# Performance work log

Measured on AMD Instinct MI355X. Metric: run time of the kernel, lower is better.

## Reference

```python
import jax, jax.numpy as jnp
import numpy as np

N = 100000   # total nodes (types a: [0,50000), b: [50000,100000))
E = 500000   # edges per edge type
T = 4        # number of edge types
D_IN = 128
H = 4        # heads
F = 32       # out_feats per head
NEG_SLOPE = 0.2


def setup_inputs() -> dict:
    key = jax.random.key(0)
    ks = jax.random.split(key, 8)
    feat = jax.random.normal(ks[0], (N, D_IN), dtype=jnp.float32)
    src = jax.random.randint(ks[1], (T, E), 0, N)
    dst = jax.random.randint(ks[2], (T, E), 0, N)
    is_b = jnp.arange(N) >= (N // 2)  # node-type mask (type2mask)
    W = jax.random.normal(ks[3], (T, D_IN, H * F), dtype=jnp.float32) * (1.0 / np.sqrt(D_IN))
    attn_l = jax.random.normal(ks[4], (T, H, F), dtype=jnp.float32) * 0.1
    attn_r = jax.random.normal(ks[5], (T, H, F), dtype=jnp.float32) * 0.1
    W_merge = jax.random.normal(ks[6], (2 * H * F, F), dtype=jnp.float32) * (1.0 / np.sqrt(2 * H * F))
    b_merge = jax.random.normal(ks[7], (F,), dtype=jnp.float32) * 0.01
    return {"feat": feat, "src": src, "dst": dst, "is_b": is_b,
            "W": W, "attn_l": attn_l, "attn_r": attn_r,
            "W_merge": W_merge, "b_merge": b_merge}


def _gat_etype(feat, src_t, dst_t, W_t, al_t, ar_t):
    # Projected features: [N, H, F]
    ft = (feat @ W_t).reshape(N, H, F)
    el = jnp.einsum('nhf,hf->nh', ft, al_t)  # [N, H]
    er = jnp.einsum('nhf,hf->nh', ft, ar_t)  # [N, H]
    # u_add_v then LeakyReLU: [E, H]
    e = el[src_t] + er[dst_t]
    e = jnp.where(e > 0, e, NEG_SLOPE * e)
    # edge_softmax over incoming edges of each dst node (stable)
    m = jax.lax.stop_gradient(jax.ops.segment_max(e, dst_t, num_segments=N))
    ex = jnp.exp(e - m[dst_t])
    denom = jax.ops.segment_sum(ex, dst_t, num_segments=N)
    a = ex / denom[dst_t]  # [E, H]
    # u_mul_e + scatter-sum: [N, H, F]
    msg = ft[src_t] * a[:, :, None]
    out = jax.ops.segment_sum(msg, dst_t, num_segments=N)
    return out.reshape(N, H * F)


def reference(feat, src, dst, is_b, W, attn_l, attn_r, W_merge, b_merge):
    outs = [_gat_etype(feat, src[t], dst[t], W[t], attn_l[t], attn_r[t])
            for t in range(T)]
    # etypes dst order: a, a, b, b -> two per-etype feats per dst ntype
    feat_a = jnp.concatenate([outs[0], outs[1]], axis=1) @ W_merge + b_merge  # [N, F]
    feat_b = jnp.concatenate([outs[2], outs[3]], axis=1) @ W_merge + b_merge  # [N, F]
    # base_aggr_func: start with type-a result, overwrite type-b rows
    return jnp.where(is_b[:, None], feat_b, feat_a)
```

## Files before the change

kernel.cpp:

```cpp
#include <hip/hip_runtime.h>
#include <hip/hip_fp16.h>

typedef short short8 __attribute__((ext_vector_type(8)));
typedef _Float16 half8 __attribute__((ext_vector_type(8)));
typedef float f32x4 __attribute__((ext_vector_type(4)));

#define N_NODES 100000
#define N_A     50000
#define N_EDGES 500000
#define N_T     4
#define D_IN    128
#define HF      128
#define BCOLS   144
#define TN      (N_T * N_NODES)
#define TE      (N_T * N_EDGES)
#define NB1     ((TN + 1023) / 1024)
#define TILE_E  (BCOLS * D_IN)
#define LOG2E   1.44269504088896340736f
#define NPROJB  1563
#define NHISTB  ((TE + 255) / 256)

__device__ __forceinline__ unsigned short f2b(float f) {
  unsigned int u = __float_as_uint(f);
  u += 0x7FFFu + ((u >> 16) & 1u);
  return (unsigned short)(u >> 16);
}
__device__ __forceinline__ unsigned int pkh(float lo, float hi) {
  auto v = __builtin_amdgcn_cvt_pkrtz(lo, hi);
  unsigned int u; __builtin_memcpy(&u, &v, 4); return u;
}
__device__ __forceinline__ unsigned short f2h(float f) {
  auto v = __builtin_amdgcn_cvt_pkrtz(f, 0.f);
  unsigned int u; __builtin_memcpy(&u, &v, 4); return (unsigned short)(u & 0xFFFFu);
}
__device__ __forceinline__ __half2 w2h(unsigned int u) {
  __half2 h; __builtin_memcpy(&h, &u, 4); return h;
}
__device__ __forceinline__ unsigned int h2w(__half2 h) {
  unsigned int u; __builtin_memcpy(&u, &h, 4); return u;
}

__global__ __launch_bounds__(256) void k_prep(const float* __restrict__ W,
    const float* __restrict__ al, const float* __restrict__ ar,
    const float* __restrict__ Wm,
    unsigned short* __restrict__ Bt, unsigned short* __restrict__ WmT)
{
  if (blockIdx.x < 2) {
    int idx = blockIdx.x * 256 + threadIdx.x;
    int t = idx >> 7, k = idx & 127;
    const float* Wr = W + ((size_t)t * D_IN + k) * HF;
    unsigned short* o = Bt + (size_t)t * TILE_E;
    for (int j = 0; j < HF; ++j)
      o[(j * D_IN + k) ^ ((j & 7) << 3)] = f2b(Wr[j]);
    for (int h = 0; h < 4; ++h) {
      float sl = 0.f, sr = 0.f;
      const float* alh = al + (t * 4 + h) * 32;
      const float* arh = ar + (t * 4 + h) * 32;
      for (int f = 0; f < 32; ++f) { float w = Wr[h * 32 + f]; sl += w * alh[f]; sr += w * arh[f]; }
      int jl = 128 + h, jr = 132 + h;
      o[(jl * D_IN + k) ^ ((jl & 7) << 3)] = f2b(sl * LOG2E);
      o[(jr * D_IN + k) ^ ((jr & 7) << 3)] = f2b(sr * LOG2E);
    }
    for (int j = 136; j < 144; ++j)
      o[(j * D_IN + k) ^ ((j & 7) << 3)] = 0;
  } else {
    int idx = (blockIdx.x - 2) * 256 + threadIdx.x;
    int kidx = idx >> 5, j = idx & 31;
    int slot = kidx >> 7, p = kidx & 127;
    int col = (p & 7) * 16 + (p >> 3);
    WmT[j * 256 + kidx] = f2h(Wm[(slot * 128 + col) * 32 + j]);
  }
}

__global__ __launch_bounds__(256, 4) void k_projhist(const float* __restrict__ feat,
    const unsigned short* __restrict__ Btg,
    unsigned short* __restrict__ ftg,
    float* __restrict__ elg, float* __restrict__ erg,
    const int* __restrict__ dst, int* __restrict__ cnt, int* __restrict__ rank)
{
  if (blockIdx.x >= NPROJB) {
    int idx = (blockIdx.x - NPROJB) * 256 + threadIdx.x;
    if (idx >= TE) return;
    int t = idx / N_EDGES;
    int d = dst[idx];
    bool keep = (t < 2) ? (d < N_A) : (d >= N_A);
    if (keep) rank[idx] = atomicAdd(&cnt[t * N_NODES + d], 1);
    return;
  }
  __shared__ __align__(16) unsigned short Bs[TILE_E];
  const int tid = threadIdx.x;
  const int wave = tid >> 6, lane = tid & 63;
  const int l15 = lane & 15, g = lane >> 4;
  const int wrow0 = blockIdx.x * 64 + wave * 16;

  short8 a[4];
  {
    int row = wrow0 + l15;
    const float* fr = feat + (size_t)(row < N_NODES ? row : N_NODES - 1) * D_IN;
#pragma unroll
    for (int kt = 0; kt < 4; ++kt) {
      float4 v0 = *(const float4*)(fr + kt * 32 + g * 8);
      float4 v1 = *(const float4*)(fr + kt * 32 + g * 8 + 4);
      short8 s;
      s[0] = (short)f2b(v0.x); s[1] = (short)f2b(v0.y);
      s[2] = (short)f2b(v0.z); s[3] = (short)f2b(v0.w);
      s[4] = (short)f2b(v1.x); s[5] = (short)f2b(v1.y);
      s[6] = (short)f2b(v1.z); s[7] = (short)f2b(v1.w);
      a[kt] = s;
    }
  }

  for (int t = 0; t < N_T; ++t) {
    if (t > 0) __syncthreads();
    {
      const uint4* src = (const uint4*)(Btg + (size_t)t * TILE_E);
      uint4* dstv = (uint4*)Bs;
#pragma unroll
      for (int i = 0; i < 9; ++i)
        dstv[i * 256 + tid] = src[i * 256 + tid];
    }
    __syncthreads();

    f32x4 acc[8];
#pragma unroll
    for (int ct = 0; ct < 8; ++ct) {
      f32x4 c = {0.f, 0.f, 0.f, 0.f};
#pragma unroll
      for (int kt = 0; kt < 4; ++kt) {
        int row = ct * 16 + l15;
        int boff = (row * 256 + kt * 64 + g * 16) ^ ((l15 & 7) << 4);
        short8 b = *(const short8*)((const char*)Bs + boff);
        c = __builtin_amdgcn_mfma_f32_16x16x32_bf16(a[kt], b, c, 0, 0, 0);
      }
      acc[ct] = c;
    }
    {
      f32x4 c8 = {0.f, 0.f, 0.f, 0.f};
#pragma unroll
      for (int kt = 0; kt < 4; ++kt) {
        int row = 128 + l15;
        int boff = (row * 256 + kt * 64 + g * 16) ^ ((l15 & 7) << 4);
        short8 b = *(const short8*)((const char*)Bs + boff);
        c8 = __builtin_amdgcn_mfma_f32_16x16x32_bf16(a[kt], b, c8, 0, 0, 0);
      }
      if (l15 < 8) {
#pragma unroll
        for (int r = 0; r < 4; ++r) {
          int row = wrow0 + g * 4 + r;
          if (row < N_NODES) {
            float v = c8[r];
            if (l15 < 4) elg[((size_t)t * N_NODES + row) * 4 + l15] = v;
            else         erg[((size_t)t * N_NODES + row) * 4 + (l15 - 4)] = v;
          }
        }
      }
    }
#pragma unroll
    for (int r = 0; r < 4; ++r) {
      int row = wrow0 + g * 4 + r;
      if (row < N_NODES) {
        uint4 o;
        o.x = pkh(acc[0][r], acc[1][r]);
        o.y = pkh(acc[2][r], acc[3][r]);
        o.z = pkh(acc[4][r], acc[5][r]);
        o.w = pkh(acc[6][r], acc[7][r]);
        *(uint4*)(ftg + ((size_t)t * N_NODES + row) * HF + l15 * 8) = o;
      }
    }
  }
}

__global__ __launch_bounds__(256) void k_scan1(const int* __restrict__ cnt,
    int* __restrict__ ofs, int* __restrict__ bsum) {
  __shared__ int ts[256];
  int b = blockIdx.x, t = threadIdx.x;
  int base = b * 1024 + t * 4;
  int v0 = 0, v1 = 0, v2 = 0, v3 = 0;
  if (base + 0 < TN) v0 = cnt[base + 0];
  if (base + 1 < TN) v1 = cnt[base + 1];
  if (base + 2 < TN) v2 = cnt[base + 2];
  if (base + 3 < TN) v3 = cnt[base + 3];
  int s = v0 + v1 + v2 + v3;
  ts[t] = s;
  __syncthreads();
  for (int o = 1; o < 256; o <<= 1) {
    int x = (t >= o) ? ts[t - o] : 0;
    __syncthreads();
    ts[t] += x;
    __syncthreads();
  }
  int run = ts[t] - s;
  if (base + 0 < TN) ofs[base + 0] = run; run += v0;
  if (base + 1 < TN) ofs[base + 1] = run; run += v1;
  if (base + 2 < TN) ofs[base + 2] = run; run += v2;
  if (base + 3 < TN) ofs[base + 3] = run;
  if (t == 255) bsum[b] = ts[255];
}

__global__ __launch_bounds__(512) void k_scan2(int* __restrict__ bsum) {
  __shared__ int ts[512];
  int t = threadIdx.x;
  int v = (t < NB1) ? bsum[t] : 0;
  ts[t] = v;
  __syncthreads();
  for (int o = 1; o < 512; o <<= 1) {
    int x = (t >= o) ? ts[t - o] : 0;
    __syncthreads();
    ts[t] += x;
    __syncthreads();
  }
  if (t < NB1) bsum[t] = ts[t] - v;
}

__global__ __launch_bounds__(256) void k_scatter(const int* __restrict__ src, const int* __restrict__ dst,
    const int* __restrict__ ofs, const int* __restrict__ bsum, const int* __restrict__ rank,
    int* __restrict__ bkt) {
  int idx = blockIdx.x * 256 + threadIdx.x;
  if (idx >= TE) return;
  int t = idx / N_EDGES;
  int d = dst[idx];
  bool keep = (t < 2) ? (d < N_A) : (d >= N_A);
  if (!keep) return;
  int key = t * N_NODES + d;
  int p = ofs[key] + bsum[key >> 10] + rank[idx];
  bkt[p] = t * N_NODES + src[idx];
}

__global__ __launch_bounds__(256) void k_gather(const int* __restrict__ bkt,
    const int* __restrict__ ofs, const int* __restrict__ cnt, const int* __restrict__ bsum,
    const float* __restrict__ elg, const float* __restrict__ erg,
    const uint4* __restrict__ ftu, uint4* __restrict__ aggb)
{
  int wid = blockIdx.x * 4 + (threadIdx.x >> 6);
  int lane = threadIdx.x & 63;
  int g8 = lane >> 3, l7 = lane & 7;
  int pid = wid * 8 + g8;
  int n = pid >> 1, slot = pid & 1;
  int t = slot + ((n >= N_A) ? 2 : 0);
  int key = t * N_NODES + n;
  int base = ofs[key] + bsum[key >> 10];
  int c = cnt[key];
  float4 er4 = *(const float4*)(erg + (size_t)key * 4);
  __half2 A0 = __float2half2_rn(0.f), A1 = A0, A2 = A0, A3 = A0;
  __half2 B0 = A0, B1 = A0, B2 = A0, B3 = A0;
  float d0 = 0.f, d1 = 0.f, d2 = 0.f, d3 = 0.f;
  int qb = l7 * 2;
  for (int i = 0; i < c; i += 4) {
    bool v1 = i + 1 < c, v2 = i + 2 < c, v3 = i + 3 < c;
    int e0 = base + i;
    int e1 = base + (v1 ? i + 1 : i);
    int e2 = base + (v2 ? i + 2 : i);
    int e3 = base + (v3 ? i + 3 : i);
    int s0 = bkt[e0], s1 = bkt[e1], s2 = bkt[e2], s3 = bkt[e3];
    float4 eA = *(const float4*)(elg + (size_t)s0 * 4);
    float4 eB = *(const float4*)(elg + (size_t)s1 * 4);
    float4 eC = *(const float4*)(elg + (size_t)s2 * 4);
    float4 eD = *(const float4*)(elg + (size_t)s3 * 4);
    uint4 u0a = ftu[(size_t)s0 * 16 + qb], u0b = ftu[(size_t)s0 * 16 + qb + 1];
    uint4 u1a = ftu[(size_t)s1 * 16 + qb], u1b = ftu[(size_t)s1 * 16 + qb + 1];
    uint4 u2a = ftu[(size_t)s2 * 16 + qb], u2b = ftu[(size_t)s2 * 16 + qb + 1];
    uint4 u3a = ftu[(size_t)s3 * 16 + qb], u3b = ftu[(size_t)s3 * 16 + qb + 1];
    float s;
    float wa0, wa1, wa2, wa3, wb0, wb1, wb2, wb3;
    float wc0, wc1, wc2, wc3, wd0, wd1, wd2, wd3;
    s = eA.x + er4.x; wa0 = exp2f(fmaxf(s, 0.2f * s));
    s = eA.y + er4.y; wa1 = exp2f(fmaxf(s, 0.2f * s));
    s = eA.z + er4.z; wa2 = exp2f(fmaxf(s, 0.2f * s));
    s = eA.w + er4.w; wa3 = exp2f(fmaxf(s, 0.2f * s));
    s = eB.x + er4.x; wb0 = exp2f(fmaxf(s, 0.2f * s));
    s = eB.y + er4.y; wb1 = exp2f(fmaxf(s, 0.2f * s));
    s = eB.z + er4.z; wb2 = exp2f(fmaxf(s, 0.2f * s));
    s = eB.w + er4.w; wb3 = exp2f(fmaxf(s, 0.2f * s));
    s = eC.x + er4.x; wc0 = exp2f(fmaxf(s, 0.2f * s));
    s = eC.y + er4.y; wc1 = exp2f(fmaxf(s, 0.2f * s));
    s = eC.z + er4.z; wc2 = exp2f(fmaxf(s, 0.2f * s));
    s = eC.w + er4.w; wc3 = exp2f(fmaxf(s, 0.2f * s));
    s = eD.x + er4.x; wd0 = exp2f(fmaxf(s, 0.2f * s));
    s = eD.y + er4.y; wd1 = exp2f(fmaxf(s, 0.2f * s));
    s = eD.z + er4.z; wd2 = exp2f(fmaxf(s, 0.2f * s));
    s = eD.w + er4.w; wd3 = exp2f(fmaxf(s, 0.2f * s));
    if (!v1) { wb0 = wb1 = wb2 = wb3 = 0.f; }
    if (!v2) { wc0 = wc1 = wc2 = wc3 = 0.f; }
    if (!v3) { wd0 = wd1 = wd2 = wd3 = 0.f; }
    d0 += wa0 + wb0 + wc0 + wd0;
    d1 += wa1 + wb1 + wc1 + wd1;
    d2 += wa2 + wb2 + wc2 + wd2;
    d3 += wa3 + wb3 + wc3 + wd3;
    __half2 h0, h1, h2, h3;
    h0 = __float2half2_rn(wa0); h1 = __float2half2_rn(wa1);
    h2 = __float2half2_rn(wa2); h3 = __float2half2_rn(wa3);
    A0 = __hfma2(w2h(u0a.x), h0, A0); A1 = __hfma2(w2h(u0a.y), h1, A1);
    A2 = __hfma2(w2h(u0a.z), h2, A2); A3 = __hfma2(w2h(u0a.w), h3, A3);
    B0 = __hfma2(w2h(u0b.x), h0, B0); B1 = __hfma2(w2h(u0b.y), h1, B1);
    B2 = __hfma2(w2h(u0b.z), h2, B2); B3 = __hfma2(w2h(u0b.w), h3, B3);
    h0 = __float2half2_rn(wb0); h1 = __float2half2_rn(wb1);
    h2 = __float2half2_rn(wb2); h3 = __float2half2_rn(wb3);
    A0 = __hfma2(w2h(u1a.x), h0, A0); A1 = __hfma2(w2h(u1a.y), h1, A1);
    A2 = __hfma2(w2h(u1a.z), h2, A2); A3 = __hfma2(w2h(u1a.w), h3, A3);
    B0 = __hfma2(w2h(u1b.x), h0, B0); B1 = __hfma2(w2h(u1b.y), h1, B1);
    B2 = __hfma2(w2h(u1b.z), h2, B2); B3 = __hfma2(w2h(u1b.w), h3, B3);
    h0 = __float2half2_rn(wc0); h1 = __float2half2_rn(wc1);
    h2 = __float2half2_rn(wc2); h3 = __float2half2_rn(wc3);
    A0 = __hfma2(w2h(u2a.x), h0, A0); A1 = __hfma2(w2h(u2a.y), h1, A1);
    A2 = __hfma2(w2h(u2a.z), h2, A2); A3 = __hfma2(w2h(u2a.w), h3, A3);
    B0 = __hfma2(w2h(u2b.x), h0, B0); B1 = __hfma2(w2h(u2b.y), h1, B1);
    B2 = __hfma2(w2h(u2b.z), h2, B2); B3 = __hfma2(w2h(u2b.w), h3, B3);
    h0 = __float2half2_rn(wd0); h1 = __float2half2_rn(wd1);
    h2 = __float2half2_rn(wd2); h3 = __float2half2_rn(wd3);
    A0 = __hfma2(w2h(u3a.x), h0, A0); A1 = __hfma2(w2h(u3a.y), h1, A1);
    A2 = __hfma2(w2h(u3a.z), h2, A2); A3 = __hfma2(w2h(u3a.w), h3, A3);
    B0 = __hfma2(w2h(u3b.x), h0, B0); B1 = __hfma2(w2h(u3b.y), h1, B1);
    B2 = __hfma2(w2h(u3b.z), h2, B2); B3 = __hfma2(w2h(u3b.w), h3, B3);
  }
  __half2 i0 = __float2half2_rn((c > 0) ? 1.f / d0 : 0.f);
  __half2 i1 = __float2half2_rn((c > 0) ? 1.f / d1 : 0.f);
  __half2 i2 = __float2half2_rn((c > 0) ? 1.f / d2 : 0.f);
  __half2 i3 = __float2half2_rn((c > 0) ? 1.f / d3 : 0.f);
  uint4 oA, oB;
  oA.x = h2w(__hmul2(A0, i0)); oA.y = h2w(__hmul2(A1, i1));
  oA.z = h2w(__hmul2(A2, i2)); oA.w = h2w(__hmul2(A3, i3));
  oB.x = h2w(__hmul2(B0, i0)); oB.y = h2w(__hmul2(B1, i1));
  oB.z = h2w(__hmul2(B2, i2)); oB.w = h2w(__hmul2(B3, i3));
  size_t ob = (size_t)n * 32 + slot * 16 + qb;
  aggb[ob] = oA;
  aggb[ob + 1] = oB;
}

__global__ __launch_bounds__(256) void k_merge(const unsigned short* __restrict__ aggb,
    const unsigned short* __restrict__ WmT, const float* __restrict__ bm,
    float* __restrict__ out)
{
  __shared__ __align__(16) unsigned short Al[64 * 264];
  __shared__ __align__(16) unsigned short Bl[32 * 264];
  int n0 = blockIdx.x * 64;
  int tid = threadIdx.x;
  const uint4* asrc = (const uint4*)(aggb + (size_t)n0 * 256);
  for (int i = tid; i < 2048; i += 256) {
    int r = i >> 5, c = i & 31;
    *(uint4*)&Al[r * 264 + c * 8] = asrc[r * 32 + c];
  }
  for (int i = tid; i < 1024; i += 256) {
    int r = i >> 5, c = i & 31;
    *(uint4*)&Bl[r * 264 + c * 8] = ((const uint4*)WmT)[r * 32 + c];
  }
  __syncthreads();
  int wave = tid >> 6, lane = tid & 63;
  int l15 = lane & 15, lk = (lane >> 4) * 8;
  half8 a[8];
#pragma unroll
  for (int kt = 0; kt < 8; ++kt)
    a[kt] = *(const half8*)&Al[(wave * 16 + l15) * 264 + kt * 32 + lk];
  f32x4 acc0 = {0.f, 0.f, 0.f, 0.f}, acc1 = {0.f, 0.f, 0.f, 0.f};
#pragma unroll
  for (int kt = 0; kt < 8; ++kt) {
    half8 b0 = *(const half8*)&Bl[l15 * 264 + kt * 32 + lk];
    half8 b1 = *(const half8*)&Bl[(16 + l15) * 264 + kt * 32 + lk];
    acc0 = __builtin_amdgcn_mfma_f32_16x16x32_f16(a[kt], b0, acc0, 0, 0, 0);
    acc1 = __builtin_amdgcn_mfma_f32_16x16x32_f16(a[kt], b1, acc1, 0, 0, 0);
  }
  float bm0 = bm[l15], bm1 = bm[16 + l15];
#pragma unroll
  for (int r = 0; r < 4; ++r) {
    int row = n0 + wave * 16 + (lane >> 4) * 4 + r;
    if (row < N_NODES) {
      out[(size_t)row * 32 + l15] = acc0[r] + bm0;
      out[(size_t)row * 32 + 16 + l15] = acc1[r] + bm1;
    }
  }
}

extern "C" void kernel_launch(void* const* d_in, const int* in_sizes, int n_in,
                              void* d_out, int out_size, void* d_ws, size_t ws_size,
                              hipStream_t stream)
{
  const float* feat = (const float*)d_in[0];
  const int*   src  = (const int*)d_in[1];
  const int*   dst  = (const int*)d_in[2];
  const float* W    = (const float*)d_in[4];
  const float* al   = (const float*)d_in[5];
  const float* ar   = (const float*)d_in[6];
  const float* Wm   = (const float*)d_in[7];
  const float* bm   = (const float*)d_in[8];
  float* out = (float*)d_out;
  (void)in_sizes; (void)n_in; (void)out_size; (void)ws_size;

  char* w = (char*)d_ws;
  size_t o = 0;
  auto take = [&](size_t bytes) -> void* {
    void* p = w + o;
    o += (bytes + 255) & ~(size_t)255;
    return p;
  };
  unsigned short* Btg = (unsigned short*)take((size_t)N_T * TILE_E * 2);
  unsigned short* WmT = (unsigned short*)take((size_t)32 * 256 * 2);
  unsigned short* ftg = (unsigned short*)take((size_t)N_T * N_NODES * HF * 2);
  float* elg   = (float*)take((size_t)N_T * N_NODES * 4 * 4);
  float* erg   = (float*)take((size_t)N_T * N_NODES * 4 * 4);
  int*   cntb  = (int*)take((size_t)TN * 4);
  int*   ofs   = (int*)take((size_t)TN * 4);
  int*   bsum  = (int*)take(4096);
  int*   rank  = (int*)take((size_t)TE * 4);
  int*   bkt   = (int*)take((size_t)TE * 4);
  unsigned short* aggb = (unsigned short*)take((size_t)(N_NODES + 64) * 256 * 2);

  hipMemsetAsync(cntb, 0, (size_t)TN * 4, stream);

  k_prep<<<34, 256, 0, stream>>>(W, al, ar, Wm, Btg, WmT);
  k_projhist<<<NPROJB + NHISTB, 256, 0, stream>>>(feat, Btg, ftg, elg, erg, dst, cntb, rank);
  k_scan1<<<NB1, 256, 0, stream>>>(cntb, ofs, bsum);
  k_scan2<<<1, 512, 0, stream>>>(bsum);
  k_scatter<<<(TE + 255) / 256, 256, 0, stream>>>(src, dst, ofs, bsum, rank, bkt);
  k_gather<<<6250, 256, 0, stream>>>(bkt, ofs, cntb, bsum, elg, erg, (const uint4*)ftg, (uint4*)aggb);
  k_merge<<<1563, 256, 0, stream>>>(aggb, WmT, bm, out);
}
```

Before: 197.2 us.

## Fuse merge GEMM into gather kernel and split projection from histogram

The merge matmul now runs inside the gather kernel. Each block stages its 16 aggregated node rows in LDS and two waves apply the merge MFMA with weights read directly from global memory, so the intermediate aggregate buffer is never written or reread. The combined projection/histogram launch is split into two separate kernels. This gives up the overlap between the two and leaves half the waves idle during the merge step.

```diff
diff --git a/kernel.cpp b/kernel.cpp
--- a/kernel.cpp
+++ b/kernel.cpp
@@ -17,8 +17,6 @@
 #define NB1     ((TN + 1023) / 1024)
 #define TILE_E  (BCOLS * D_IN)
 #define LOG2E   1.44269504088896340736f
-#define NPROJB  1563
-#define NHISTB  ((TE + 255) / 256)
 
 __device__ __forceinline__ unsigned short f2b(float f) {
   unsigned int u = __float_as_uint(f);
@@ -72,21 +70,11 @@
   }
 }
 
-__global__ __launch_bounds__(256, 4) void k_projhist(const float* __restrict__ feat,
+__global__ __launch_bounds__(256, 4) void k_proj(const float* __restrict__ feat,
     const unsigned short* __restrict__ Btg,
     unsigned short* __restrict__ ftg,
-    float* __restrict__ elg, float* __restrict__ erg,
-    const int* __restrict__ dst, int* __restrict__ cnt, int* __restrict__ rank)
+    float* __restrict__ elg, float* __restrict__ erg)
 {
-  if (blockIdx.x >= NPROJB) {
-    int idx = (blockIdx.x - NPROJB) * 256 + threadIdx.x;
-    if (idx >= TE) return;
-    int t = idx / N_EDGES;
-    int d = dst[idx];
-    bool keep = (t < 2) ? (d < N_A) : (d >= N_A);
-    if (keep) rank[idx] = atomicAdd(&cnt[t * N_NODES + d], 1);
-    return;
-  }
   __shared__ __align__(16) unsigned short Bs[TILE_E];
   const int tid = threadIdx.x;
   const int wave = tid >> 6, lane = tid & 63;
@@ -168,6 +156,16 @@
       }
     }
   }
+}
+
+__global__ __launch_bounds__(256) void k_hist(const int* __restrict__ dst,
+    int* __restrict__ cnt, int* __restrict__ rank) {
+  int idx = blockIdx.x * 256 + threadIdx.x;
+  if (idx >= TE) return;
+  int t = idx / N_EDGES;
+  int d = dst[idx];
+  bool keep = (t < 2) ? (d < N_A) : (d >= N_A);
+  if (keep) rank[idx] = atomicAdd(&cnt[t * N_NODES + d], 1);
 }
 
 __global__ __launch_bounds__(256) void k_scan1(const int* __restrict__ cnt,
@@ -226,15 +224,19 @@
   bkt[p] = t * N_NODES + src[idx];
 }
 
-__global__ __launch_bounds__(256) void k_gather(const int* __restrict__ bkt,
+__global__ __launch_bounds__(256) void k_gathermerge(const int* __restrict__ bkt,
     const int* __restrict__ ofs, const int* __restrict__ cnt, const int* __restrict__ bsum,
     const float* __restrict__ elg, const float* __restrict__ erg,
-    const uint4* __restrict__ ftu, uint4* __restrict__ aggb)
+    const uint4* __restrict__ ftu,
+    const unsigned short* __restrict__ WmT, const float* __restrict__ bm,
+    float* __restrict__ out)
 {
-  int wid = blockIdx.x * 4 + (threadIdx.x >> 6);
-  int lane = threadIdx.x & 63;
+  __shared__ __align__(16) unsigned short Al[16 * 264];
+  int tid = threadIdx.x;
+  int wave = tid >> 6, lane = tid & 63;
   int g8 = lane >> 3, l7 = lane & 7;
-  int pid = wid * 8 + g8;
+  int pidl = wave * 8 + g8;
+  int pid = blockIdx.x * 32 + pidl;
   int n = pid >> 1, slot = pid & 1;
   int t = slot + ((n >= N_A) ? 2 : 0);
   int key = t * N_NODES + n;
@@ -321,51 +323,25 @@
   oA.z = h2w(__hmul2(A2, i2)); oA.w = h2w(__hmul2(A3, i3));
   oB.x = h2w(__hmul2(B0, i0)); oB.y = h2w(__hmul2(B1, i1));
   oB.z = h2w(__hmul2(B2, i2)); oB.w = h2w(__hmul2(B3, i3));
-  size_t ob = (size_t)n * 32 + slot * 16 + qb;
-  aggb[ob] = oA;
-  aggb[ob + 1] = oB;
-}
-
-__global__ __launch_bounds__(256) void k_merge(const unsigned short* __restrict__ aggb,
-    const unsigned short* __restrict__ WmT, const float* __restrict__ bm,
-    float* __restrict__ out)
-{
-  __shared__ __align__(16) unsigned short Al[64 * 264];
-  __shared__ __align__(16) unsigned short Bl[32 * 264];
-  int n0 = blockIdx.x * 64;
-  int tid = threadIdx.x;
-  const uint4* asrc = (const uint4*)(aggb + (size_t)n0 * 256);
-  for (int i = tid; i < 2048; i += 256) {
-    int r = i >> 5, c = i & 31;
-    *(uint4*)&Al[r * 264 + c * 8] = asrc[r * 32 + c];
-  }
-  for (int i = tid; i < 1024; i += 256) {
-    int r = i >> 5, c = i & 31;
-    *(uint4*)&Bl[r * 264 + c * 8] = ((const uint4*)WmT)[r * 32 + c];
-  }
+  int nl = pidl >> 1;
+  *(uint4*)&Al[nl * 264 + slot * 128 + l7 * 16] = oA;
+  *(uint4*)&Al[nl * 264 + slot * 128 + l7 * 16 + 8] = oB;
   __syncthreads();
-  int wave = tid >> 6, lane = tid & 63;
+  if (wave >= 2) return;
+
   int l15 = lane & 15, lk = (lane >> 4) * 8;
-  half8 a[8];
-#pragma unroll
-  for (int kt = 0; kt < 8; ++kt)
-    a[kt] = *(const half8*)&Al[(wave * 16 + l15) * 264 + kt * 32 + lk];
-  f32x4 acc0 = {0.f, 0.f, 0.f, 0.f}, acc1 = {0.f, 0.f, 0.f, 0.f};
+  f32x4 acc = {0.f, 0.f, 0.f, 0.f};
 #pragma unroll
   for (int kt = 0; kt < 8; ++kt) {
-    half8 b0 = *(const half8*)&Bl[l15 * 264 + kt * 32 + lk];
-    half8 b1 = *(const half8*)&Bl[(16 + l15) * 264 + kt * 32 + lk];
-    acc0 = __builtin_amdgcn_mfma_f32_16x16x32_f16(a[kt], b0, acc0, 0, 0, 0);
-    acc1 = __builtin_amdgcn_mfma_f32_16x16x32_f16(a[kt], b1, acc1, 0, 0, 0);
-  }
-  float bm0 = bm[l15], bm1 = bm[16 + l15];
+    half8 a = *(const half8*)&Al[l15 * 264 + kt * 32 + lk];
+    half8 b = *(const half8*)(const void*)(WmT + (size_t)(wave * 16 + l15) * 256 + kt * 32 + lk);
+    acc = __builtin_amdgcn_mfma_f32_16x16x32_f16(a, b, acc, 0, 0, 0);
+  }
+  float bmv = bm[wave * 16 + l15];
 #pragma unroll
   for (int r = 0; r < 4; ++r) {
-    int row = n0 + wave * 16 + (lane >> 4) * 4 + r;
-    if (row < N_NODES) {
-      out[(size_t)row * 32 + l15] = acc0[r] + bm0;
-      out[(size_t)row * 32 + 16 + l15] = acc1[r] + bm1;
-    }
+    int row = blockIdx.x * 16 + (lane >> 4) * 4 + r;
+    out[(size_t)row * 32 + wave * 16 + l15] = acc[r] + bmv;
   }
 }
 
@@ -401,15 +377,15 @@
   int*   bsum  = (int*)take(4096);
   int*   rank  = (int*)take((size_t)TE * 4);
   int*   bkt   = (int*)take((size_t)TE * 4);
-  unsigned short* aggb = (unsigned short*)take((size_t)(N_NODES + 64) * 256 * 2);
 
   hipMemsetAsync(cntb, 0, (size_t)TN * 4, stream);
 
   k_prep<<<34, 256, 0, stream>>>(W, al, ar, Wm, Btg, WmT);
-  k_projhist<<<NPROJB + NHISTB, 256, 0, stream>>>(feat, Btg, ftg, elg, erg, dst, cntb, rank);
+  k_proj<<<1563, 256, 0, stream>>>(feat, Btg, ftg, elg, erg);
+  k_hist<<<(TE + 255) / 256, 256, 0, stream>>>(dst, cntb, rank);
   k_scan1<<<NB1, 256, 0, stream>>>(cntb, ofs, bsum);
   k_scan2<<<1, 512, 0, stream>>>(bsum);
   k_scatter<<<(TE + 255) / 256, 256, 0, stream>>>(src, dst, ofs, bsum, rank, bkt);
-  k_gather<<<6250, 256, 0, stream>>>(bkt, ofs, cntb, bsum, elg, erg, (const uint4*)ftg, (uint4*)aggb);
-  k_merge<<<1563, 256, 0, stream>>>(aggb, WmT, bm, out);
-}
+  k_gathermerge<<<6250, 256, 0, stream>>>(bkt, ofs, cntb, bsum, elg, erg,
+                                          (const uint4*)ftg, WmT, bm, out);
+}
```

Result: faster. 187.7 us (-4.8%).
